# Kernel tuning notes

Hardware: AMD Instinct MI355X
Metric: run time of the kernel (lower is better)

## Reference

```python
import jax, jax.numpy as jnp
import numpy as np

BN_EPS = 1e-5

# Binary activation with hardtanh STE semantics (forward: sign)
@jax.custom_vjp
def binary_act(x):
    return jnp.sign(x)

def _ba_fwd(x):
    return jnp.sign(x), x

def _ba_bwd(x, g):
    return (jnp.where(jnp.abs(x) > 1.0, 0.0, g),)

binary_act.defvjp(_ba_fwd, _ba_bwd)

# Binary weight quantizer (forward: sign, backward: identity STE)
@jax.custom_vjp
def binary_w(x):
    return jnp.sign(x)

def _bw_fwd(x):
    return jnp.sign(x), None

def _bw_bwd(_, g):
    return (g,)

binary_w.defvjp(_bw_fwd, _bw_bwd)


def setup_inputs() -> dict:
    key = jax.random.key(0)
    k1, k2, k3 = jax.random.split(key, 3)
    B, C_in, H, W_sp = 32, 256, 56, 56
    C_out, KH, KW = 256, 3, 3
    x = jax.random.normal(k1, (B, C_in, H, W_sp), dtype=jnp.float32)
    weight = jax.random.normal(k2, (C_out, C_in, KH, KW), dtype=jnp.float32) * 0.05
    bias = jax.random.normal(k3, (C_out,), dtype=jnp.float32) * 0.01
    gamma = jnp.ones((C_out,), dtype=jnp.float32)
    beta = jnp.zeros((C_out,), dtype=jnp.float32)
    return {"x": x, "weight": weight, "bias": bias, "gamma": gamma, "beta": beta}


def reference(x, weight, bias, gamma, beta):
    # --- activation binarization (A=2): sign ---
    xb = binary_act(x)
    # --- weight binarization (W=2): mean-center over in-channel dim, clamp, sign * alpha ---
    wc = weight - jnp.mean(weight, axis=1, keepdims=True)
    wc = jnp.clip(wc, -1.0, 1.0)
    alpha = jnp.mean(jnp.abs(wc), axis=(1, 2, 3), keepdims=True)  # per-output-channel scale
    wq = binary_w(wc) * alpha
    # --- conv2d, stride 1, padding 1 ---
    y = jax.lax.conv_general_dilated(
        xb, wq, window_strides=(1, 1), padding=((1, 1), (1, 1)),
        dimension_numbers=("NCHW", "OIHW", "NCHW"))
    y = y + bias[None, :, None, None]
    # --- BatchNorm2d (training-mode batch statistics, biased variance) ---
    mu = jnp.mean(y, axis=(0, 2, 3), keepdims=True)
    var = jnp.var(y, axis=(0, 2, 3), keepdims=True)
    y = (y - mu) * jax.lax.rsqrt(var + BN_EPS)
    y = y * gamma[None, :, None, None] + beta[None, :, None, None]
    # --- last_relu=1 ---
    y = jax.nn.relu(y)
    # --- last_bin=1 (A=2 -> binary activation) ---
    y = binary_act(y)
    return y
```

## Files before the change

kernel.cpp:

```cpp
#include <hip/hip_runtime.h>

typedef unsigned long long u64;
typedef int i32x4 __attribute__((ext_vector_type(4)));
typedef int i32x16 __attribute__((ext_vector_type(16)));

#define N_SP 3136
#define C_IN 256
#define C_OUT 256
#define BATCH 32
#define NBLK 1792
#define XROW 64
#define XPLANE (58 * XROW * 256)
#define XSIZE ((size_t)BATCH * XPLANE)

__global__ __launch_bounds__(256) void prep_weights(const float* __restrict__ w,
                                                    char* __restrict__ A_pack,
                                                    double* __restrict__ alpha) {
    const int o = blockIdx.x;
    const int i = threadIdx.x;
    const int lane = i & 63, wvid = i >> 6;
    __shared__ double part[4][9];
    __shared__ double part2[4];

    float wv[9];
    const float* wp = w + ((size_t)o * C_IN + i) * 9;
#pragma unroll
    for (int t = 0; t < 9; ++t) wv[t] = wp[t];

#pragma unroll
    for (int t = 0; t < 9; ++t) {
        double v = (double)wv[t];
#pragma unroll
        for (int off = 32; off > 0; off >>= 1) v += __shfl_down(v, off);
        if (lane == 0) part[wvid][t] = v;
    }
    __syncthreads();

    double asum = 0.0;
#pragma unroll
    for (int t = 0; t < 9; ++t) {
        double mean = (part[0][t] + part[1][t] + part[2][t] + part[3][t]) * (1.0 / 256.0);
        double wc = (double)wv[t] - mean;
        int idx16 = ((t * 8 + (i >> 5)) * 8 + (o >> 5)) * 64 + (((i >> 4) & 1) << 5) + (o & 31);
        A_pack[(size_t)idx16 * 16 + (i & 15)] = (char)(wc > 0.0 ? 1 : -1);
        double aw = fabs(wc);
        if (aw > 1.0) aw = 1.0;
        asum += aw;
    }
#pragma unroll
    for (int off = 32; off > 0; off >>= 1) asum += __shfl_down(asum, off);
    if (lane == 0) part2[wvid] = asum;
    __syncthreads();
    if (i == 0)
        alpha[o] = (part2[0] + part2[1] + part2[2] + part2[3]) * (1.0 / 2304.0);
}

__global__ __launch_bounds__(256) void zero_borders(char* __restrict__ xsT) {
    const int tid = blockIdx.x * 256 + threadIdx.x;
    const int b = tid / 9216;
    const int r = tid - b * 9216;
    int hp, wp, c16;
    if (r < 2048) {
        hp = (r >> 10) * 57;
        wp = (r >> 4) & 63;
        c16 = (r & 15) << 4;
    } else {
        int r2 = r - 2048;
        hp = 1 + (r2 >> 7);
        int q = r2 & 127;
        int wi = q >> 4;
        wp = (wi == 0) ? 0 : 56 + wi;
        c16 = (q & 15) << 4;
    }
    *(i32x4*)(xsT + (((size_t)(b * 58 + hp) << 6) + wp) * 256 + c16) = (i32x4){0, 0, 0, 0};
}

__global__ __launch_bounds__(256) void sign_transpose(const float* __restrict__ x,
                                                      char* __restrict__ xsT) {
    const int sp0 = blockIdx.x * 64;
    const int b = blockIdx.y;
    const int lane = threadIdx.x & 63;
    const int wv = threadIdx.x >> 6;
    __shared__ char tile[64 * 272];

    const float* xp = x + ((size_t)(b * 256 + (wv << 6))) * N_SP + sp0 + lane;
#pragma unroll
    for (int q = 0; q < 4; ++q) {
        unsigned d[4];
#pragma unroll
        for (int dd = 0; dd < 4; ++dd) {
            unsigned v = 0;
#pragma unroll
            for (int kk = 0; kk < 4; ++kk) {
                int ci_l = (q << 4) + (dd << 2) + kk;
                float xv = xp[(size_t)ci_l * N_SP];
                v |= (unsigned)(xv > 0.0f ? 0x01u : 0xFFu) << (8 * kk);
            }
            d[dd] = v;
        }
        *(i32x4*)(tile + lane * 272 + (wv << 6) + (q << 4)) =
            (i32x4){(int)d[0], (int)d[1], (int)d[2], (int)d[3]};
    }
    __syncthreads();

    const int t = threadIdx.x;
#pragma unroll
    for (int j = 0; j < 4; ++j) {
        int sp_loc = (j << 4) + (t >> 4);
        int ci0 = (t & 15) << 4;
        i32x4 v = *(const i32x4*)(tile + sp_loc * 272 + ci0);
        int spg = sp0 + sp_loc;
        int h = spg / 56, w = spg - h * 56;
        size_t dst = (((size_t)(b * 58 + h + 1) << 6) + (w + 1)) * 256 + ci0;
        *(i32x4*)(xsT + dst) = v;
    }
}

__global__ __launch_bounds__(256, 3) void conv_mfma(const char* __restrict__ xsT,
                                                    const char* __restrict__ A_pack,
                                                    float* __restrict__ out,
                                                    int2* __restrict__ partials) {
    const int tid = threadIdx.x;
    const int lane = tid & 63;
    const int wv = tid >> 6;
    const int l31 = lane & 31, l5 = lane >> 5;
    const int blk = blockIdx.x;
    const int b = blk / 56;
    const int h0 = blk - b * 56;

    __shared__ char slab[3 * 58 * 272];

    {
        const char* src = xsT + ((size_t)(b * 58 + h0) << 6) * 256;
        for (int c = tid; c < 3 * 58 * 16; c += 256) {
            int dh = c / (58 * 16);
            int rem = c - dh * (58 * 16);
            int wp = rem >> 4, c16 = (rem & 15) << 4;
            *(i32x4*)(slab + (dh * 58 + wp) * 272 + c16) =
                *(const i32x4*)(src + (size_t)dh * (XROW * 256) + wp * 256 + c16);
        }
    }
    __syncthreads();

    i32x16 acc[2][2] = {};

#pragma unroll
    for (int tap = 0; tap < 9; ++tap) {
        const int dh = tap / 3, dw = tap % 3;
        const char* s0 = slab + (dh * 58 + (l31 + dw)) * 272 + l5 * 16;
        int w1 = 32 + l31 + dw;
        if (w1 > 57) w1 = 57;
        const char* s1 = slab + (dh * 58 + w1) * 272 + l5 * 16;
        const char* ap = A_pack + ((size_t)((tap * 8) * 8 + 2 * wv) * 64 + lane) * 16;
#pragma unroll
        for (int cib = 0; cib < 8; ++cib) {
            i32x4 a0 = *(const i32x4*)(ap + (size_t)cib * 8192);
            i32x4 a1 = *(const i32x4*)(ap + (size_t)cib * 8192 + 1024);
            i32x4 b0 = *(const i32x4*)(s0 + cib * 32);
            i32x4 b1 = *(const i32x4*)(s1 + cib * 32);
            acc[0][0] = __builtin_amdgcn_mfma_i32_32x32x32_i8(a0, b0, acc[0][0], 0, 0, 0);
            acc[0][1] = __builtin_amdgcn_mfma_i32_32x32x32_i8(a0, b1, acc[0][1], 0, 0, 0);
            acc[1][0] = __builtin_amdgcn_mfma_i32_32x32x32_i8(a1, b0, acc[1][0], 0, 0, 0);
            acc[1][1] = __builtin_amdgcn_mfma_i32_32x32x32_i8(a1, b1, acc[1][1], 0, 0, 0);
        }
    }

    float* ob = out + ((size_t)(b * 256)) * N_SP + h0 * 56;
#pragma unroll
    for (int co_i = 0; co_i < 2; ++co_i) {
        const int co5 = 2 * wv + co_i;
#pragma unroll
        for (int nh = 0; nh < 2; ++nh) {
            const int w = nh * 32 + l31;
            if (w < 56) {
#pragma unroll
                for (int reg = 0; reg < 16; ++reg) {
                    int corow = (reg & 3) + 8 * (reg >> 2) + 4 * l5;
                    ob[(size_t)(co5 * 32 + corow) * N_SP + w] = (float)acc[co_i][nh][reg];
                }
            }
        }
    }

    __syncthreads();
    int* sp_s = (int*)slab;
    int* sp_q = (int*)slab + 256;
#pragma unroll
    for (int co_i = 0; co_i < 2; ++co_i) {
#pragma unroll
        for (int reg = 0; reg < 16; ++reg) {
            int v0 = acc[co_i][0][reg];
            int v1 = (l31 < 24) ? acc[co_i][1][reg] : 0;
            int s = v0 + v1;
            unsigned q = (unsigned)(v0 * v0) + (unsigned)(v1 * v1);
#pragma unroll
            for (int off = 16; off > 0; off >>= 1) {
                s += __shfl_xor(s, off);
                q += (unsigned)__shfl_xor((int)q, off);
            }
            if (l31 == 0) {
                int corow = (reg & 3) + 8 * (reg >> 2) + 4 * l5;
                sp_s[(2 * wv + co_i) * 32 + corow] = s;
                sp_q[(2 * wv + co_i) * 32 + corow] = (int)q;
            }
        }
    }
    __syncthreads();
    partials[(size_t)tid * NBLK + blk] = make_int2(sp_s[tid], sp_q[tid]);
}

__global__ __launch_bounds__(256) void stats_consts(const int2* __restrict__ partials,
                                                    const double* __restrict__ alpha,
                                                    const float* __restrict__ gamma,
                                                    const float* __restrict__ beta,
                                                    double* __restrict__ AB) {
    const int c = blockIdx.x;
    const int t = threadIdx.x;
    long long s1 = 0, s2 = 0;
    for (int blk = t; blk < NBLK; blk += 256) {
        int2 v = partials[(size_t)c * NBLK + blk];
        s1 += v.x;
        s2 += (long long)v.y;
    }
#pragma unroll
    for (int off = 32; off > 0; off >>= 1) {
        s1 += __shfl_down(s1, off);
        s2 += __shfl_down(s2, off);
    }
    __shared__ long long p1[4], p2[4];
    if ((t & 63) == 0) { p1[t >> 6] = s1; p2[t >> 6] = s2; }
    __syncthreads();
    if (t == 0) {
        double S1 = (double)(p1[0] + p1[1] + p1[2] + p1[3]);
        double S2 = (double)(p2[0] + p2[1] + p2[2] + p2[3]);
        const double N = (double)(BATCH * N_SP);
        double mu = S1 / N;
        double var = S2 / N - mu * mu;
        double a = alpha[c];
        double vy = a * a * var;
        double scale = (double)gamma[c] / sqrt(vy + 1e-5);
        double A = a * scale;
        double B = (double)beta[c] - A * mu;
        AB[c] = A;
        AB[C_OUT + c] = B;
    }
}

__global__ __launch_bounds__(256) void finalize(float* __restrict__ out,
                                                const double* __restrict__ AB) {
    const unsigned i4 = blockIdx.x * 256 + threadIdx.x;
    const unsigned e = i4 << 2;
    const int c = (int)((e / N_SP) & (C_OUT - 1));
    const double A = AB[c];
    const double B = AB[C_OUT + c];
    float4 v = ((float4*)out)[i4];
    v.x = (A * (double)v.x + B) > 0.0 ? 1.0f : 0.0f;
    v.y = (A * (double)v.y + B) > 0.0 ? 1.0f : 0.0f;
    v.z = (A * (double)v.z + B) > 0.0 ? 1.0f : 0.0f;
    v.w = (A * (double)v.w + B) > 0.0 ? 1.0f : 0.0f;
    ((float4*)out)[i4] = v;
}

extern "C" void kernel_launch(void* const* d_in, const int* in_sizes, int n_in,
                              void* d_out, int out_size, void* d_ws, size_t ws_size,
                              hipStream_t stream) {
    const float* x      = (const float*)d_in[0];
    const float* weight = (const float*)d_in[1];
    const float* bias   = (const float*)d_in[2];   (void)bias;
    const float* gamma  = (const float*)d_in[3];
    const float* beta   = (const float*)d_in[4];
    float* out = (float*)d_out;

    char* ws = (char*)d_ws;
    double* alpha = (double*)(ws + 4096);
    double* AB    = (double*)(ws + 8192);
    char*   A_pack = (char*)(ws + 16384);
    int2*   partials = (int2*)(ws + (1 << 20));
    char*   xsT   = (char*)(ws + (5 << 20));

    prep_weights<<<C_OUT, 256, 0, stream>>>(weight, A_pack, alpha);
    zero_borders<<<1152, 256, 0, stream>>>(xsT);
    sign_transpose<<<dim3(49, BATCH), 256, 0, stream>>>(x, xsT);
    conv_mfma<<<dim3(NBLK), 256, 0, stream>>>(xsT, A_pack, out, partials);
    stats_consts<<<C_OUT, 256, 0, stream>>>(partials, alpha, gamma, beta, AB);
    finalize<<<(out_size / 4) / 256, 256, 0, stream>>>(out, AB);
}
```

Before: 322.6 us.

## Compute two output rows per conv block and fuse border zeroing into transpose

Each conv block now covers two output rows, loading a four-row input slab so each weight fragment feeds eight MFMAs instead of four. This halves global weight-fragment loads per output and halves the number of blocks. The border-zeroing kernel is merged into sign_transpose to drop a launch. In exchange it uses more accumulator registers and LDS, and occupancy is lowered to 2 blocks per CU.

```diff
diff --git a/kernel.cpp b/kernel.cpp
--- a/kernel.cpp
+++ b/kernel.cpp
@@ -8,7 +8,7 @@
 #define C_IN 256
 #define C_OUT 256
 #define BATCH 32
-#define NBLK 1792
+#define NBLK 896
 #define XROW 64
 #define XPLANE (58 * XROW * 256)
 #define XSIZE ((size_t)BATCH * XPLANE)
@@ -55,26 +55,6 @@
         alpha[o] = (part2[0] + part2[1] + part2[2] + part2[3]) * (1.0 / 2304.0);
 }
 
-__global__ __launch_bounds__(256) void zero_borders(char* __restrict__ xsT) {
-    const int tid = blockIdx.x * 256 + threadIdx.x;
-    const int b = tid / 9216;
-    const int r = tid - b * 9216;
-    int hp, wp, c16;
-    if (r < 2048) {
-        hp = (r >> 10) * 57;
-        wp = (r >> 4) & 63;
-        c16 = (r & 15) << 4;
-    } else {
-        int r2 = r - 2048;
-        hp = 1 + (r2 >> 7);
-        int q = r2 & 127;
-        int wi = q >> 4;
-        wp = (wi == 0) ? 0 : 56 + wi;
-        c16 = (q & 15) << 4;
-    }
-    *(i32x4*)(xsT + (((size_t)(b * 58 + hp) << 6) + wp) * 256 + c16) = (i32x4){0, 0, 0, 0};
-}
-
 __global__ __launch_bounds__(256) void sign_transpose(const float* __restrict__ x,
                                                       char* __restrict__ xsT) {
     const int sp0 = blockIdx.x * 64;
@@ -82,6 +62,29 @@
     const int lane = threadIdx.x & 63;
     const int wv = threadIdx.x >> 6;
     __shared__ char tile[64 * 272];
+
+    {
+        const int tidl = (blockIdx.y * 49 + blockIdx.x) * 256 + threadIdx.x;
+        if (tidl < 294912) {
+            const int bb = tidl / 9216;
+            const int r = tidl - bb * 9216;
+            int hp, wp, c16;
+            if (r < 2048) {
+                hp = (r >> 10) * 57;
+                wp = (r >> 4) & 63;
+                c16 = (r & 15) << 4;
+            } else {
+                int r2 = r - 2048;
+                hp = 1 + (r2 >> 7);
+                int q = r2 & 127;
+                int wi = q >> 4;
+                wp = (wi == 0) ? 0 : 56 + wi;
+                c16 = (q & 15) << 4;
+            }
+            *(i32x4*)(xsT + (((size_t)(bb * 58 + hp) << 6) + wp) * 256 + c16) =
+                (i32x4){0, 0, 0, 0};
+        }
+    }
 
     const float* xp = x + ((size_t)(b * 256 + (wv << 6))) * N_SP + sp0 + lane;
 #pragma unroll
@@ -116,7 +119,7 @@
     }
 }
 
-__global__ __launch_bounds__(256, 3) void conv_mfma(const char* __restrict__ xsT,
+__global__ __launch_bounds__(256, 2) void conv_mfma(const char* __restrict__ xsT,
                                                     const char* __restrict__ A_pack,
                                                     float* __restrict__ out,
                                                     int2* __restrict__ partials) {
@@ -125,14 +128,14 @@
     const int wv = tid >> 6;
     const int l31 = lane & 31, l5 = lane >> 5;
     const int blk = blockIdx.x;
-    const int b = blk / 56;
-    const int h0 = blk - b * 56;
-
-    __shared__ char slab[3 * 58 * 272];
+    const int b = blk / 28;
+    const int h0 = (blk - b * 28) * 2;
+
+    __shared__ char slab[4 * 58 * 272];
 
     {
         const char* src = xsT + ((size_t)(b * 58 + h0) << 6) * 256;
-        for (int c = tid; c < 3 * 58 * 16; c += 256) {
+        for (int c = tid; c < 4 * 58 * 16; c += 256) {
             int dh = c / (58 * 16);
             int rem = c - dh * (58 * 16);
             int wp = rem >> 4, c16 = (rem & 15) << 4;
@@ -142,26 +145,38 @@
     }
     __syncthreads();
 
-    i32x16 acc[2][2] = {};
+    i32x16 acc[2][2][2] = {};
+
+    const char* apb = A_pack + ((size_t)(2 * wv * 64 + lane)) * 16;
+    const char* sb0 = slab + l31 * 272 + l5 * 16;
+    int w1_0 = 32 + l31;     if (w1_0 > 57) w1_0 = 57;
+    int w1_1 = 33 + l31;     if (w1_1 > 57) w1_1 = 57;
+    int w1_2 = 34 + l31;     if (w1_2 > 57) w1_2 = 57;
+    const char* sb1_0 = slab + w1_0 * 272 + l5 * 16;
+    const char* sb1_1 = slab + w1_1 * 272 + l5 * 16;
+    const char* sb1_2 = slab + w1_2 * 272 + l5 * 16;
 
 #pragma unroll
     for (int tap = 0; tap < 9; ++tap) {
-        const int dh = tap / 3, dw = tap % 3;
-        const char* s0 = slab + (dh * 58 + (l31 + dw)) * 272 + l5 * 16;
-        int w1 = 32 + l31 + dw;
-        if (w1 > 57) w1 = 57;
-        const char* s1 = slab + (dh * 58 + w1) * 272 + l5 * 16;
-        const char* ap = A_pack + ((size_t)((tap * 8) * 8 + 2 * wv) * 64 + lane) * 16;
+        const int dh = tap / 3, dw = tap - 3 * (tap / 3);
+        const char* sb1 = (dw == 0) ? sb1_0 : ((dw == 1) ? sb1_1 : sb1_2);
 #pragma unroll
         for (int cib = 0; cib < 8; ++cib) {
-            i32x4 a0 = *(const i32x4*)(ap + (size_t)cib * 8192);
-            i32x4 a1 = *(const i32x4*)(ap + (size_t)cib * 8192 + 1024);
-            i32x4 b0 = *(const i32x4*)(s0 + cib * 32);
-            i32x4 b1 = *(const i32x4*)(s1 + cib * 32);
-            acc[0][0] = __builtin_amdgcn_mfma_i32_32x32x32_i8(a0, b0, acc[0][0], 0, 0, 0);
-            acc[0][1] = __builtin_amdgcn_mfma_i32_32x32x32_i8(a0, b1, acc[0][1], 0, 0, 0);
-            acc[1][0] = __builtin_amdgcn_mfma_i32_32x32x32_i8(a1, b0, acc[1][0], 0, 0, 0);
-            acc[1][1] = __builtin_amdgcn_mfma_i32_32x32x32_i8(a1, b1, acc[1][1], 0, 0, 0);
+            const int it = tap * 8 + cib;
+            i32x4 a0 = *(const i32x4*)(apb + (size_t)it * 8192);
+            i32x4 a1 = *(const i32x4*)(apb + (size_t)it * 8192 + 1024);
+            i32x4 b00 = *(const i32x4*)(sb0 + ((dh + 0) * 58 + dw) * 272 + cib * 32);
+            i32x4 b01 = *(const i32x4*)(sb0 + ((dh + 1) * 58 + dw) * 272 + cib * 32);
+            i32x4 b10 = *(const i32x4*)(sb1 + (dh + 0) * 58 * 272 + cib * 32);
+            i32x4 b11 = *(const i32x4*)(sb1 + (dh + 1) * 58 * 272 + cib * 32);
+            acc[0][0][0] = __builtin_amdgcn_mfma_i32_32x32x32_i8(a0, b00, acc[0][0][0], 0, 0, 0);
+            acc[0][0][1] = __builtin_amdgcn_mfma_i32_32x32x32_i8(a0, b01, acc[0][0][1], 0, 0, 0);
+            acc[0][1][0] = __builtin_amdgcn_mfma_i32_32x32x32_i8(a0, b10, acc[0][1][0], 0, 0, 0);
+            acc[0][1][1] = __builtin_amdgcn_mfma_i32_32x32x32_i8(a0, b11, acc[0][1][1], 0, 0, 0);
+            acc[1][0][0] = __builtin_amdgcn_mfma_i32_32x32x32_i8(a1, b00, acc[1][0][0], 0, 0, 0);
+            acc[1][0][1] = __builtin_amdgcn_mfma_i32_32x32x32_i8(a1, b01, acc[1][0][1], 0, 0, 0);
+            acc[1][1][0] = __builtin_amdgcn_mfma_i32_32x32x32_i8(a1, b10, acc[1][1][0], 0, 0, 0);
+            acc[1][1][1] = __builtin_amdgcn_mfma_i32_32x32x32_i8(a1, b11, acc[1][1][1], 0, 0, 0);
         }
     }
 
@@ -174,10 +189,13 @@
             const int w = nh * 32 + l31;
             if (w < 56) {
 #pragma unroll
-                for (int reg = 0; reg < 16; ++reg) {
-                    int corow = (reg & 3) + 8 * (reg >> 2) + 4 * l5;
-                    ob[(size_t)(co5 * 32 + corow) * N_SP + w] = (float)acc[co_i][nh][reg];
-                }
+                for (int row = 0; row < 2; ++row)
+#pragma unroll
+                    for (int reg = 0; reg < 16; ++reg) {
+                        int corow = (reg & 3) + 8 * (reg >> 2) + 4 * l5;
+                        ob[(size_t)(co5 * 32 + corow) * N_SP + row * 56 + w] =
+                            (float)acc[co_i][nh][row][reg];
+                    }
             }
         }
     }
@@ -189,10 +207,12 @@
     for (int co_i = 0; co_i < 2; ++co_i) {
 #pragma unroll
         for (int reg = 0; reg < 16; ++reg) {
-            int v0 = acc[co_i][0][reg];
-            int v1 = (l31 < 24) ? acc[co_i][1][reg] : 0;
-            int s = v0 + v1;
-            unsigned q = (unsigned)(v0 * v0) + (unsigned)(v1 * v1);
+            int v00 = acc[co_i][0][0][reg], v01 = acc[co_i][0][1][reg];
+            int v10 = (l31 < 24) ? acc[co_i][1][0][reg] : 0;
+            int v11 = (l31 < 24) ? acc[co_i][1][1][reg] : 0;
+            int s = v00 + v01 + v10 + v11;
+            unsigned q = (unsigned)(v00 * v00) + (unsigned)(v01 * v01)
+                       + (unsigned)(v10 * v10) + (unsigned)(v11 * v11);
 #pragma unroll
             for (int off = 16; off > 0; off >>= 1) {
                 s += __shfl_xor(s, off);
@@ -279,7 +299,6 @@
     char*   xsT   = (char*)(ws + (5 << 20));
 
     prep_weights<<<C_OUT, 256, 0, stream>>>(weight, A_pack, alpha);
-    zero_borders<<<1152, 256, 0, stream>>>(xsT);
     sign_transpose<<<dim3(49, BATCH), 256, 0, stream>>>(x, xsT);
     conv_mfma<<<dim3(NBLK), 256, 0, stream>>>(xsT, A_pack, out, partials);
     stats_consts<<<C_OUT, 256, 0, stream>>>(partials, alpha, gamma, beta, AB);
```

New measurement: 357.0 us. +10.7%, slower.
